# Kernel optimization log

Measured on AMD Instinct MI355X. Metric: run time of the kernel, lower is better.

Reference implementation:

```python
import jax, jax.numpy as jnp
import numpy as np

EPS = 1e-5
GROUPS = 4
KSZ = 3
PAD = 1
CUTON = 0.1


def conv1x1(x, w):
    # x: [b,c,h,w], w: [o,c,1,1]
    return jnp.einsum('bchw,oc->bohw', x, w[:, :, 0, 0])


def bn_eval(x, g, b, m, v):
    scale = g / jnp.sqrt(v + EPS)
    return (x - m[None, :, None, None]) * scale[None, :, None, None] + b[None, :, None, None]


def extract_patches(xp, k):
    # xp: [b,c,H+2p,W+2p] -> [b,c,h,w,k,k] (matches torch unfold(2,k,1).unfold(3,k,1))
    h = xp.shape[2] - k + 1
    w = xp.shape[3] - k + 1
    p = jnp.stack([xp[:, :, i:i + h, j:j + w] for i in range(k) for j in range(k)], axis=-1)
    return p.reshape(p.shape[:-1] + (k, k))


def batch_fftshift(z):
    # faithful to roll_n with n = d//2 (+1 if odd), over dims 1..3; roll_n == roll by -n
    for ax in (1, 2, 3):
        d = z.shape[ax]
        z = jnp.roll(z, -(d // 2 + (d % 2)), axis=ax)
    return z


def batch_ifftshift(z):
    for ax in (3, 2, 1):
        z = jnp.roll(z, -(z.shape[ax] // 2), axis=ax)
    return z


def attention_conv(x, yq, q_w, k_w, v_w, rel_h, rel_w):
    b, c, h, w = x.shape
    C = q_w.shape[0]
    px = jnp.pad(x, ((0, 0), (0, 0), (PAD, PAD), (PAD, PAD)))
    q = conv1x1(yq, q_w)                      # [b,C,h,w]
    k = conv1x1(px, k_w)
    v = conv1x1(px, v_w)
    kp = extract_patches(k, KSZ)              # [b,C,h,w,3,3]
    vp = extract_patches(v, KSZ)
    kh, kw = kp[:, :C // 2], kp[:, C // 2:]
    kp = jnp.concatenate([kh + rel_h, kw + rel_w], axis=1)
    kp = kp.reshape(b, GROUPS, C // GROUPS, h, w, KSZ * KSZ)
    vp = vp.reshape(b, GROUPS, C // GROUPS, h, w, KSZ * KSZ)
    q = q.reshape(b, GROUPS, C // GROUPS, h, w, 1)
    attn = jax.nn.softmax(q * kp, axis=-1)
    out = jnp.einsum('bgchwk,bgchwk->bgchw', attn, vp)
    return out.reshape(b, C, h, w)


def fam(x, rate1, rate2, w1, w0_w, w0_b):
    h, w = x.shape[2], x.shape[3]
    # torch.fft.fftn with dim=None -> FFT over ALL dims (batch & channel too)
    x_ft = jnp.fft.fftn(x, norm='ortho')
    out_ft = jnp.einsum('bixy,ioxy->boxy', x_ft, w1)
    s = batch_fftshift(out_ft)
    cy, cx = h // 2, w // 2
    rh, rw = int(CUTON * cy), int(CUTON * cx)
    mask = jnp.ones((h, w), dtype=x.dtype).at[cy - rh:cy + rh, cx - rw:cx + rw].set(0.0)
    s = s * mask
    out_ft = batch_ifftshift(s)
    # torch.fft.ifftn with s=(h,w) -> inverse FFT over last two dims only
    out = jnp.fft.ifftn(out_ft, s=(h, w), norm='ortho').real
    out2 = conv1x1(x, w0_w) + w0_b[None, :, None, None]
    return rate1 * out + rate2 * out2


def setup_inputs() -> dict:
    key = jax.random.key(0)
    ks = jax.random.split(key, 16)
    B, Cx, Cy, M, O, H, W = 4, 128, 256, 128, 128, 64, 64
    scale = 1.0 / (M * O)
    inp = {
        'x': jax.random.normal(ks[0], (B, Cx, H, W), jnp.float32),
        'y': jax.random.normal(ks[1], (B, Cy, H // 2, W // 2), jnp.float32),
        'conv1_w': jax.random.normal(ks[2], (M, Cy, 1, 1), jnp.float32) * 0.05,
        'bn1_g': jnp.ones((M,), jnp.float32),
        'bn1_b': jnp.zeros((M,), jnp.float32),
        'bn1_m': jnp.zeros((M,), jnp.float32),
        'bn1_v': jnp.ones((M,), jnp.float32),
        'q_w': jax.random.normal(ks[3], (M, M, 1, 1), jnp.float32) * 0.05,
        'k_w': jax.random.normal(ks[4], (M, M, 1, 1), jnp.float32) * 0.05,
        'v_w': jax.random.normal(ks[5], (M, M, 1, 1), jnp.float32) * 0.05,
        'rel_h': jax.random.normal(ks[6], (M // 2, 1, 1, 3, 1), jnp.float32),
        'rel_w': jax.random.normal(ks[7], (M // 2, 1, 1, 1, 3), jnp.float32),
        'rate1': jnp.full((1,), 0.5, jnp.float32),
        'rate2': jnp.full((1,), 0.5, jnp.float32),
        'w1_real': scale * jax.random.uniform(ks[8], (M, O, H, W), jnp.float32),
        'w1_imag': scale * jax.random.uniform(ks[9], (M, O, H, W), jnp.float32),
        'w0_w': jax.random.normal(ks[10], (O, M, 1, 1), jnp.float32) * 0.05,
        'w0_b': jnp.zeros((O,), jnp.float32),
        'bn2_g': jnp.ones((O,), jnp.float32),
        'bn2_b': jnp.zeros((O,), jnp.float32),
        'bn2_m': jnp.zeros((O,), jnp.float32),
        'bn2_v': jnp.ones((O,), jnp.float32),
    }
    return inp


def reference(x, y, conv1_w, bn1_g, bn1_b, bn1_m, bn1_v, q_w, k_w, v_w, rel_h, rel_w,
              rate1, rate2, w1_real, w1_imag, w0_w, w0_b, bn2_g, bn2_b, bn2_m, bn2_v):
    # conv1 (teacher proj) + BN + ReLU
    y1 = jax.nn.relu(bn_eval(conv1x1(y, conv1_w), bn1_g, bn1_b, bn1_m, bn1_v))
    # nearest interpolate to x spatial size (torch 'nearest': idx = floor(i*in/out))
    H, W = x.shape[2], x.shape[3]
    ih = (jnp.arange(H) * y1.shape[2]) // H
    iw = (jnp.arange(W) * y1.shape[3]) // W
    y_up = y1[:, :, ih][:, :, :, iw]
    # local unfold attention
    x_att = attention_conv(x, y_up, q_w, k_w, v_w, rel_h, rel_w)
    # FAM spectral branch + BN + ReLU
    w1 = jax.lax.complex(w1_real, w1_imag)
    y_out = jax.nn.relu(bn_eval(fam(x_att, rate1, rate2, w1, w0_w, w0_b),
                                bn2_g, bn2_b, bn2_m, bn2_v))
    return (y_out, x_att)
```

## Files before the change

### kernel.cpp

```cpp
#include <hip/hip_runtime.h>

#define BB 4
#define CY 256
#define CM 128
#define HW 4096
#define HWy 1024
#define PHW 4356
#define EPSF 1e-5f
#define TWOPI 6.2831853071795864769f

struct c32 { float re, im; };


__global__ void conv1_kernel(const float* __restrict__ y, const float* __restrict__ w,
                             const float* __restrict__ g, const float* __restrict__ bb,
                             const float* __restrict__ m, const float* __restrict__ v,
                             float* __restrict__ y1){
  int p = blockIdx.x*256 + threadIdx.x;
  int ocb = blockIdx.y*8;
  int b = blockIdx.z;
  float acc[8] = {0,0,0,0,0,0,0,0};
  const float* yb = y + (size_t)b*CY*HWy + p;
  #pragma unroll 4
  for(int ic=0; ic<CY; ic++){
    float xv = yb[(size_t)ic*HWy];
    #pragma unroll
    for(int j=0;j<8;j++) acc[j] += xv * w[(ocb+j)*CY + ic];
  }
  #pragma unroll
  for(int j=0;j<8;j++){
    int oc = ocb+j;
    float s = g[oc]*rsqrtf(v[oc]+EPSF);
    float bi = bb[oc] - m[oc]*s;
    float r = acc[j]*s + bi;
    y1[((size_t)(b*CM+oc))*HWy + p] = r>0.f?r:0.f;
  }
}

__global__ void qconv_kernel(const float* __restrict__ y1, const float* __restrict__ w,
                             float* __restrict__ q){
  int p = blockIdx.x*256 + threadIdx.x;
  int ocb = blockIdx.y*8; int b = blockIdx.z;
  int mi = ((p>>7)<<5) + ((p&63)>>1);
  float acc[8] = {0,0,0,0,0,0,0,0};
  const float* yb = y1 + (size_t)b*CM*HWy + mi;
  #pragma unroll 4
  for(int ic=0; ic<CM; ic++){
    float xv = yb[(size_t)ic*HWy];
    #pragma unroll
    for(int j=0;j<8;j++) acc[j] += xv * w[(ocb+j)*CM+ic];
  }
  #pragma unroll
  for(int j=0;j<8;j++) q[((size_t)(b*CM+ocb+j))*HW + p] = acc[j];
}

__global__ void kvconv_kernel(const float* __restrict__ x, const float* __restrict__ kw,
                              const float* __restrict__ vw,
                              float* __restrict__ k, float* __restrict__ v){
  int p = blockIdx.x*256 + threadIdx.x;
  int ocb = blockIdx.y*8; int b = blockIdx.z;
  if(p >= PHW) return;
  int hh = p/66, ww2 = p - hh*66;
  int ih = hh-1, iw = ww2-1;
  bool inb = (ih>=0 && ih<64 && iw>=0 && iw<64);
  float acck[8] = {0,0,0,0,0,0,0,0};
  float accv[8] = {0,0,0,0,0,0,0,0};
  if(inb){
    const float* xb = x + (size_t)b*CM*HW + ih*64 + iw;
    #pragma unroll 4
    for(int ic=0; ic<CM; ic++){
      float xv = xb[(size_t)ic*HW];
      #pragma unroll
      for(int j=0;j<8;j++){ acck[j] += xv*kw[(ocb+j)*CM+ic]; accv[j] += xv*vw[(ocb+j)*CM+ic]; }
    }
  }
  #pragma unroll
  for(int j=0;j<8;j++){
    size_t o = ((size_t)(b*CM+ocb+j))*PHW + p;
    k[o]=acck[j]; v[o]=accv[j];
  }
}


__global__ void attn_kernel(const float* __restrict__ q, const float* __restrict__ k,
                            const float* __restrict__ v, const float* __restrict__ relh,
                            const float* __restrict__ relw, float* __restrict__ xatt){
  int t = blockIdx.x*256 + threadIdx.x;
  int p = t & 4095;
  int bc = t >> 12;
  int c = bc & 127;
  int h = p>>6, w2 = p&63;
  float qv = q[(size_t)bc*HW + p];
  const float* kb = k + (size_t)bc*PHW;
  const float* vb = v + (size_t)bc*PHW;
  float lg[9], vv[9];
  #pragma unroll
  for(int ti=0; ti<3; ti++){
    #pragma unroll
    for(int tj=0; tj<3; tj++){
      int idx = (h+ti)*66 + (w2+tj);
      float rel = (c<64) ? relh[c*3+ti] : relw[(c-64)*3+tj];
      float kv = kb[idx] + rel;
      lg[ti*3+tj] = qv*kv;
      vv[ti*3+tj] = vb[idx];
    }
  }
  float mx = lg[0];
  #pragma unroll
  for(int i=1;i<9;i++) mx = fmaxf(mx, lg[i]);
  float s=0.f, o=0.f;
  #pragma unroll
  for(int i=0;i<9;i++){ float e = __expf(lg[i]-mx); s += e; o += e*vv[i]; }
  xatt[t] = o/s;
}


template<int SIGN>
__device__ inline void dft8(const c32* a, c32* X){
  constexpr float C8[8] = {1.f,0.70710678118654752f,0.f,-0.70710678118654752f,
                           -1.f,-0.70710678118654752f,0.f,0.70710678118654752f};
  constexpr float S8[8] = {0.f,0.70710678118654752f,1.f,0.70710678118654752f,
                           0.f,-0.70710678118654752f,-1.f,-0.70710678118654752f};
  #pragma unroll
  for(int kk=0;kk<8;kk++){
    float xr=0.f, xi=0.f;
    #pragma unroll
    for(int n=0;n<8;n++){
      const int j=(n*kk)&7;
      const float wr = C8[j];
      const float wi = SIGN*S8[j];
      xr += a[n].re*wr - a[n].im*wi;
      xi += a[n].re*wi + a[n].im*wr;
    }
    X[kk].re=xr; X[kk].im=xi;
  }
}

template<int SIGN, bool RIN, bool ROUT>
__global__ void fft64_kernel(const float* in, float* out,
                             int l_div, int s1, int s2, int estride, float scale){
  __shared__ c32 tmp[32][65];
  int ll = threadIdx.x & 31;
  int j  = threadIdx.x >> 5;
  int l = blockIdx.x*32 + ll;
  int base = (l/l_div)*s1 + (l%l_div)*s2;
  c32 a[8];
  #pragma unroll
  for(int n1=0;n1<8;n1++){
    int e = n1*8 + j;
    if(RIN){ a[n1].re = in[base + e*estride]; a[n1].im = 0.f; }
    else { const float2* ci = (const float2*)in; float2 t2 = ci[base + e*estride]; a[n1].re=t2.x; a[n1].im=t2.y; }
  }
  c32 A[8];
  dft8<SIGN>(a, A);
  #pragma unroll
  for(int k1=0;k1<8;k1++){
    float ang = SIGN * (TWOPI/64.f) * (float)(j*k1);
    float sn, cs; __sincosf(ang, &sn, &cs);
    c32 t; t.re = A[k1].re*cs - A[k1].im*sn; t.im = A[k1].re*sn + A[k1].im*cs;
    tmp[ll][k1*8+j] = t;
  }
  __syncthreads();
  c32 bv[8];
  #pragma unroll
  for(int n2=0;n2<8;n2++) bv[n2] = tmp[ll][j*8+n2];
  c32 Y[8];
  dft8<SIGN>(bv, Y);
  #pragma unroll
  for(int k2=0;k2<8;k2++){
    int e = j + 8*k2;
    int oi = base + e*estride;
    if(ROUT) out[oi] = Y[k2].re*scale;
    else { float2* co = (float2*)out; co[oi] = make_float2(Y[k2].re*scale, Y[k2].im*scale); }
  }
}

template<int SIGN>
__global__ void fft128_kernel(float* data, float scale){
  __shared__ c32 tmp[16][129];
  int ll = threadIdx.x & 15;
  int j  = threadIdx.x >> 4;
  int l = blockIdx.x*16 + ll;
  int b = l >> 12;
  int rem = l & 4095;
  size_t base = (size_t)b*CM*HW + rem;
  float2* cd = (float2*)data;
  c32 a[8];
  #pragma unroll
  for(int n1=0;n1<8;n1++){
    float2 t2 = cd[base + (size_t)(16*n1 + j)*HW];
    a[n1].re=t2.x; a[n1].im=t2.y;
  }
  c32 A[8];
  dft8<SIGN>(a, A);
  #pragma unroll
  for(int k1=0;k1<8;k1++){
    float ang = SIGN*(TWOPI/128.f)*(float)(j*k1);
    float sn,cs; __sincosf(ang,&sn,&cs);
    c32 t; t.re = A[k1].re*cs - A[k1].im*sn; t.im = A[k1].re*sn + A[k1].im*cs;
    tmp[ll][k1*16 + j] = t;
  }
  __syncthreads();
  int k1 = j & 7, half = j >> 3;
  c32 bv[16];
  #pragma unroll
  for(int n2=0;n2<16;n2++) bv[n2] = tmp[ll][k1*16+n2];
  #pragma unroll
  for(int kk=0;kk<8;kk++){
    int k2 = half*8 + kk;
    float xr=0.f, xi=0.f;
    #pragma unroll
    for(int n2=0;n2<16;n2++){
      float ang = SIGN*(TWOPI/16.f)*(float)((n2*k2)&15);
      float sn,cs; __sincosf(ang,&sn,&cs);
      xr += bv[n2].re*cs - bv[n2].im*sn;
      xi += bv[n2].re*sn + bv[n2].im*cs;
    }
    cd[base + (size_t)(k1 + 8*k2)*HW] = make_float2(xr*scale, xi*scale);
  }
}

__global__ void einsum_kernel(const float2* __restrict__ Xf, const float* __restrict__ w1r,
                              const float* __restrict__ w1i, float2* __restrict__ OutF){
  int fl = threadIdx.x & 63;
  int ol = threadIdx.x >> 6;
  int fbase = blockIdx.y*64;
  int obase = blockIdx.x*16;
  int f = fbase + fl;
  __shared__ float2 xs[4][64];
  c32 acc[4][4];
  #pragma unroll
  for(int a1=0;a1<4;a1++)
    #pragma unroll
    for(int a2=0;a2<4;a2++){ acc[a1][a2].re=0.f; acc[a1][a2].im=0.f; }
  for(int i=0;i<CM;i++){
    __syncthreads();
    xs[ol][fl] = Xf[((size_t)(ol*CM + i))*HW + f];
    __syncthreads();
    float2 x0=xs[0][fl], x1=xs[1][fl], x2=xs[2][fl], x3=xs[3][fl];
    c32 Xb[4];
    Xb[0].re = x0.x+x1.x+x2.x+x3.x;      Xb[0].im = x0.y+x1.y+x2.y+x3.y;
    Xb[1].re = x0.x + x1.y - x2.x - x3.y; Xb[1].im = x0.y - x1.x - x2.y + x3.x;
    Xb[2].re = x0.x - x1.x + x2.x - x3.x; Xb[2].im = x0.y - x1.y + x2.y - x3.y;
    Xb[3].re = x0.x - x1.y - x2.x + x3.y; Xb[3].im = x0.y + x1.x - x2.y - x3.x;
    #pragma unroll
    for(int oj=0;oj<4;oj++){
      int o = obase + oj*4 + ol;
      size_t wi_ = ((size_t)(i*CM + o))*HW + f;
      float wr = w1r[wi_], wim = w1i[wi_];
      #pragma unroll
      for(int kb=0;kb<4;kb++){
        acc[oj][kb].re += Xb[kb].re*wr - Xb[kb].im*wim;
        acc[oj][kb].im += Xb[kb].re*wim + Xb[kb].im*wr;
      }
    }
  }
  int hf = f>>6, wf = f&63;
  bool masked = (hf<3 || hf>60) && (wf<3 || wf>60);
  #pragma unroll
  for(int oj=0;oj<4;oj++){
    int o = obase + oj*4 + ol;
    #pragma unroll
    for(int kb=0;kb<4;kb++){
      float2 t2 = masked ? make_float2(0.f,0.f) : make_float2(acc[oj][kb].re, acc[oj][kb].im);
      OutF[((size_t)(kb*CM + o))*HW + f] = t2;
    }
  }
}

__global__ void final_kernel(const float* __restrict__ G, const float* __restrict__ xatt,
                             const float* __restrict__ w0, const float* __restrict__ w0b,
                             const float* __restrict__ r1p, const float* __restrict__ r2p,
                             const float* __restrict__ g2, const float* __restrict__ b2,
                             const float* __restrict__ m2, const float* __restrict__ v2,
                             float* __restrict__ yout){
  int p = blockIdx.x*256 + threadIdx.x;
  int ocb = blockIdx.y*8; int b = blockIdx.z;
  float r1 = r1p[0], r2 = r2p[0];
  float acc[8] = {0,0,0,0,0,0,0,0};
  const float* xb = xatt + (size_t)b*CM*HW + p;
  #pragma unroll 4
  for(int ic=0; ic<CM; ic++){
    float xv = xb[(size_t)ic*HW];
    #pragma unroll
    for(int j=0;j<8;j++) acc[j] += xv * w0[(ocb+j)*CM + ic];
  }
  #pragma unroll
  for(int j=0;j<8;j++){
    int oc = ocb+j;
    float fam = r1 * G[((size_t)(b*CM+oc))*HW + p] + r2*(acc[j] + w0b[oc]);
    float s = g2[oc]*rsqrtf(v2[oc]+EPSF);
    float bi = b2[oc] - m2[oc]*s;
    float val = fam*s + bi;
    yout[((size_t)(b*CM+oc))*HW + p] = val>0.f?val:0.f;
  }
}

extern "C" void kernel_launch(void* const* d_in, const int* in_sizes, int n_in,
                              void* d_out, int out_size, void* d_ws, size_t ws_size,
                              hipStream_t stream){
  const float* x       = (const float*)d_in[0];
  const float* y       = (const float*)d_in[1];
  const float* conv1_w = (const float*)d_in[2];
  const float* bn1_g   = (const float*)d_in[3];
  const float* bn1_b   = (const float*)d_in[4];
  const float* bn1_m   = (const float*)d_in[5];
  const float* bn1_v   = (const float*)d_in[6];
  const float* q_w     = (const float*)d_in[7];
  const float* k_w     = (const float*)d_in[8];
  const float* v_w     = (const float*)d_in[9];
  const float* rel_h   = (const float*)d_in[10];
  const float* rel_w   = (const float*)d_in[11];
  const float* rate1   = (const float*)d_in[12];
  const float* rate2   = (const float*)d_in[13];
  const float* w1r     = (const float*)d_in[14];
  const float* w1i     = (const float*)d_in[15];
  const float* w0_w    = (const float*)d_in[16];
  const float* w0_b    = (const float*)d_in[17];
  const float* bn2_g   = (const float*)d_in[18];
  const float* bn2_b   = (const float*)d_in[19];
  const float* bn2_m   = (const float*)d_in[20];
  const float* bn2_v   = (const float*)d_in[21];
  (void)in_sizes; (void)n_in; (void)out_size; (void)ws_size;

  char* ws = (char*)d_ws;
  float* Y1 = (float*)(ws + 0);
  float* Q  = (float*)(ws + 2097152);
  float* K  = (float*)(ws + 10485760);
  float* V  = (float*)(ws + 19406848);
  float2* E = (float2*)(ws + 0);
  float2* F = (float2*)(ws + 16777216);
  float*  G = (float*)(ws + 0);

  float* yout = (float*)d_out;
  float* xatt = (float*)d_out + 2097152;

  conv1_kernel<<<dim3(4,16,BB),256,0,stream>>>(y, conv1_w, bn1_g,bn1_b,bn1_m,bn1_v, Y1);
  qconv_kernel<<<dim3(16,16,BB),256,0,stream>>>(Y1, q_w, Q);
  kvconv_kernel<<<dim3(18,16,BB),256,0,stream>>>(x, k_w, v_w, K, V);
  attn_kernel<<<dim3(8192),256,0,stream>>>(Q, K, V, rel_h, rel_w, xatt);

  fft64_kernel<-1,true,false><<<dim3(1024),256,0,stream>>>(xatt, (float*)E, 64,4096,64, 1, 0.125f);
  fft64_kernel<-1,false,false><<<dim3(1024),256,0,stream>>>((float*)E, (float*)E, 64,4096,1, 64, 0.125f);
  fft128_kernel<-1><<<dim3(1024),256,0,stream>>>((float*)E, 0.044194173824159216f);
  einsum_kernel<<<dim3(8,64),256,0,stream>>>(E, w1r, w1i, F);
  fft64_kernel<1,false,false><<<dim3(1024),256,0,stream>>>((float*)F, (float*)F, 64,4096,1, 64, 0.125f);
  fft64_kernel<1,false,true><<<dim3(1024),256,0,stream>>>((float*)F, G, 64,4096,64, 1, 0.125f);

  final_kernel<<<dim3(16,16,BB),256,0,stream>>>(G, xatt, w0_w, w0_b, rate1, rate2,
                                                bn2_g,bn2_b,bn2_m,bn2_v, yout);
}
```

Measured before the change: 784.1 us.

## Fuse q-projection into attention, fuse 2D FFT passes in LDS, retile einsum

Removes the separate q-conv kernel by computing the q projection inside the attention kernel. Replaces the two separate 64-point FFT passes (forward and inverse) with one kernel per image that does both row and column FFTs in shared memory, saving global round trips. Rewrites the spectral einsum so each thread covers 4 frequencies with float4 weight loads and an 8-channel staged tile of the batch-FFT'd inputs. In exchange, attention now redoes 128-wide q dot products per thread, and the in-LDS FFT adds more syncthreads and possible bank conflicts on the strided column pass.

```diff
diff --git a/kernel.cpp b/kernel.cpp
--- a/kernel.cpp
+++ b/kernel.cpp
@@ -8,8 +8,6 @@
 #define PHW 4356
 #define EPSF 1e-5f
 #define TWOPI 6.2831853071795864769f
-
-struct c32 { float re, im; };
 
 
 __global__ void conv1_kernel(const float* __restrict__ y, const float* __restrict__ w,
@@ -35,23 +33,6 @@
     float r = acc[j]*s + bi;
     y1[((size_t)(b*CM+oc))*HWy + p] = r>0.f?r:0.f;
   }
-}
-
-__global__ void qconv_kernel(const float* __restrict__ y1, const float* __restrict__ w,
-                             float* __restrict__ q){
-  int p = blockIdx.x*256 + threadIdx.x;
-  int ocb = blockIdx.y*8; int b = blockIdx.z;
-  int mi = ((p>>7)<<5) + ((p&63)>>1);
-  float acc[8] = {0,0,0,0,0,0,0,0};
-  const float* yb = y1 + (size_t)b*CM*HWy + mi;
-  #pragma unroll 4
-  for(int ic=0; ic<CM; ic++){
-    float xv = yb[(size_t)ic*HWy];
-    #pragma unroll
-    for(int j=0;j<8;j++) acc[j] += xv * w[(ocb+j)*CM+ic];
-  }
-  #pragma unroll
-  for(int j=0;j<8;j++) q[((size_t)(b*CM+ocb+j))*HW + p] = acc[j];
 }
 
 __global__ void kvconv_kernel(const float* __restrict__ x, const float* __restrict__ kw,
@@ -82,15 +63,23 @@
 }
 
 
-__global__ void attn_kernel(const float* __restrict__ q, const float* __restrict__ k,
-                            const float* __restrict__ v, const float* __restrict__ relh,
-                            const float* __restrict__ relw, float* __restrict__ xatt){
+__global__ void attn_kernel(const float* __restrict__ y1, const float* __restrict__ qw,
+                            const float* __restrict__ k, const float* __restrict__ v,
+                            const float* __restrict__ relh, const float* __restrict__ relw,
+                            float* __restrict__ xatt){
   int t = blockIdx.x*256 + threadIdx.x;
   int p = t & 4095;
   int bc = t >> 12;
   int c = bc & 127;
+  int b = bc >> 7;
   int h = p>>6, w2 = p&63;
-  float qv = q[(size_t)bc*HW + p];
+  int mi = ((p>>7)<<5) + ((p&63)>>1);
+  const float* yb = y1 + (size_t)b*CM*HWy + mi;
+  const float* wq = qw + c*CM;
+  float qv = 0.f;
+  #pragma unroll 4
+  for(int ic=0; ic<CM; ic++) qv += yb[(size_t)ic*HWy] * wq[ic];
+
   const float* kb = k + (size_t)bc*PHW;
   const float* vb = v + (size_t)bc*PHW;
   float lg[9], vv[9];
@@ -116,7 +105,7 @@
 
 
 template<int SIGN>
-__device__ inline void dft8(const c32* a, c32* X){
+__device__ inline void dft8(const float2* a, float2* X){
   constexpr float C8[8] = {1.f,0.70710678118654752f,0.f,-0.70710678118654752f,
                            -1.f,-0.70710678118654752f,0.f,0.70710678118654752f};
   constexpr float S8[8] = {0.f,0.70710678118654752f,1.f,0.70710678118654752f,
@@ -129,55 +118,92 @@
       const int j=(n*kk)&7;
       const float wr = C8[j];
       const float wi = SIGN*S8[j];
-      xr += a[n].re*wr - a[n].im*wi;
-      xi += a[n].re*wi + a[n].im*wr;
-    }
-    X[kk].re=xr; X[kk].im=xi;
-  }
-}
-
-template<int SIGN, bool RIN, bool ROUT>
-__global__ void fft64_kernel(const float* in, float* out,
-                             int l_div, int s1, int s2, int estride, float scale){
-  __shared__ c32 tmp[32][65];
+      xr += a[n].x*wr - a[n].y*wi;
+      xi += a[n].x*wi + a[n].y*wr;
+    }
+    X[kk].x=xr; X[kk].y=xi;
+  }
+}
+
+template<int SIGN>
+__device__ inline void fft64_lds(float2* img, int lineStride, int elemStride){
+  int j  = threadIdx.x >> 5;
   int ll = threadIdx.x & 31;
-  int j  = threadIdx.x >> 5;
-  int l = blockIdx.x*32 + ll;
-  int base = (l/l_div)*s1 + (l%l_div)*s2;
-  c32 a[8];
-  #pragma unroll
-  for(int n1=0;n1<8;n1++){
-    int e = n1*8 + j;
-    if(RIN){ a[n1].re = in[base + e*estride]; a[n1].im = 0.f; }
-    else { const float2* ci = (const float2*)in; float2 t2 = ci[base + e*estride]; a[n1].re=t2.x; a[n1].im=t2.y; }
-  }
-  c32 A[8];
-  dft8<SIGN>(a, A);
-  #pragma unroll
-  for(int k1=0;k1<8;k1++){
-    float ang = SIGN * (TWOPI/64.f) * (float)(j*k1);
-    float sn, cs; __sincosf(ang, &sn, &cs);
-    c32 t; t.re = A[k1].re*cs - A[k1].im*sn; t.im = A[k1].re*sn + A[k1].im*cs;
-    tmp[ll][k1*8+j] = t;
+  #pragma unroll
+  for(int half=0; half<2; half++){
+    float2* L = img + (half*32 + ll)*lineStride;
+    float2 a[8];
+    #pragma unroll
+    for(int n1=0;n1<8;n1++) a[n1] = L[(n1*8+j)*elemStride];
+    float2 A[8];
+    dft8<SIGN>(a, A);
+    __syncthreads();
+    #pragma unroll
+    for(int k1=0;k1<8;k1++){
+      float ang = SIGN * (TWOPI/64.f) * (float)(j*k1);
+      float sn, cs; __sincosf(ang, &sn, &cs);
+      L[(k1*8+j)*elemStride] = make_float2(A[k1].x*cs - A[k1].y*sn, A[k1].x*sn + A[k1].y*cs);
+    }
+    __syncthreads();
+    float2 bv[8];
+    #pragma unroll
+    for(int n2=0;n2<8;n2++) bv[n2] = L[(j*8+n2)*elemStride];
+    float2 Y[8];
+    dft8<SIGN>(bv, Y);
+    __syncthreads();
+    #pragma unroll
+    for(int k2=0;k2<8;k2++) L[(j + 8*k2)*elemStride] = Y[k2];
+    __syncthreads();
+  }
+}
+
+__global__ void fft2d_fwd(const float* __restrict__ xatt, float2* __restrict__ E){
+  __shared__ float2 img[64*65];
+  int bc = blockIdx.x;
+  const float* src = xatt + (size_t)bc*HW;
+  for(int s=threadIdx.x; s<1024; s+=256){
+    float4 t = ((const float4*)src)[s];
+    int idx = s*4; int r = idx>>6, c = idx&63;
+    float2* d = img + r*65 + c;
+    d[0]=make_float2(t.x,0.f); d[1]=make_float2(t.y,0.f);
+    d[2]=make_float2(t.z,0.f); d[3]=make_float2(t.w,0.f);
   }
   __syncthreads();
-  c32 bv[8];
-  #pragma unroll
-  for(int n2=0;n2<8;n2++) bv[n2] = tmp[ll][j*8+n2];
-  c32 Y[8];
-  dft8<SIGN>(bv, Y);
-  #pragma unroll
-  for(int k2=0;k2<8;k2++){
-    int e = j + 8*k2;
-    int oi = base + e*estride;
-    if(ROUT) out[oi] = Y[k2].re*scale;
-    else { float2* co = (float2*)out; co[oi] = make_float2(Y[k2].re*scale, Y[k2].im*scale); }
+  fft64_lds<-1>(img, 65, 1);
+  fft64_lds<-1>(img, 1, 65);
+  float2* dst = E + (size_t)bc*HW;
+  for(int s=threadIdx.x; s<2048; s+=256){
+    int idx = s*2; int r = idx>>6, c = idx&63;
+    float2 v0 = img[r*65+c], v1 = img[r*65+c+1];
+    ((float4*)dst)[s] = make_float4(v0.x*0.015625f, v0.y*0.015625f, v1.x*0.015625f, v1.y*0.015625f);
+  }
+}
+
+__global__ void fft2d_inv(const float2* __restrict__ F, float* __restrict__ G){
+  __shared__ float2 img[64*65];
+  int bc = blockIdx.x;
+  const float2* src = F + (size_t)bc*HW;
+  for(int s=threadIdx.x; s<2048; s+=256){
+    float4 t = ((const float4*)src)[s];
+    int idx = s*2; int r = idx>>6, c = idx&63;
+    img[r*65+c]   = make_float2(t.x,t.y);
+    img[r*65+c+1] = make_float2(t.z,t.w);
+  }
+  __syncthreads();
+  fft64_lds<1>(img, 65, 1);
+  fft64_lds<1>(img, 1, 65);
+  float* dst = G + (size_t)bc*HW;
+  for(int s=threadIdx.x; s<1024; s+=256){
+    int idx = s*4; int r = idx>>6, c = idx&63;
+    float2* p2 = img + r*65 + c;
+    ((float4*)dst)[s] = make_float4(p2[0].x*0.015625f, p2[1].x*0.015625f,
+                                    p2[2].x*0.015625f, p2[3].x*0.015625f);
   }
 }
 
 template<int SIGN>
 __global__ void fft128_kernel(float* data, float scale){
-  __shared__ c32 tmp[16][129];
+  __shared__ float2 tmp[16][129];
   int ll = threadIdx.x & 15;
   int j  = threadIdx.x >> 4;
   int l = blockIdx.x*16 + ll;
@@ -185,24 +211,20 @@
   int rem = l & 4095;
   size_t base = (size_t)b*CM*HW + rem;
   float2* cd = (float2*)data;
-  c32 a[8];
-  #pragma unroll
-  for(int n1=0;n1<8;n1++){
-    float2 t2 = cd[base + (size_t)(16*n1 + j)*HW];
-    a[n1].re=t2.x; a[n1].im=t2.y;
-  }
-  c32 A[8];
+  float2 a[8];
+  #pragma unroll
+  for(int n1=0;n1<8;n1++) a[n1] = cd[base + (size_t)(16*n1 + j)*HW];
+  float2 A[8];
   dft8<SIGN>(a, A);
   #pragma unroll
   for(int k1=0;k1<8;k1++){
     float ang = SIGN*(TWOPI/128.f)*(float)(j*k1);
     float sn,cs; __sincosf(ang,&sn,&cs);
-    c32 t; t.re = A[k1].re*cs - A[k1].im*sn; t.im = A[k1].re*sn + A[k1].im*cs;
-    tmp[ll][k1*16 + j] = t;
+    tmp[ll][k1*16 + j] = make_float2(A[k1].x*cs - A[k1].y*sn, A[k1].x*sn + A[k1].y*cs);
   }
   __syncthreads();
   int k1 = j & 7, half = j >> 3;
-  c32 bv[16];
+  float2 bv[16];
   #pragma unroll
   for(int n2=0;n2<16;n2++) bv[n2] = tmp[ll][k1*16+n2];
   #pragma unroll
@@ -213,8 +235,8 @@
     for(int n2=0;n2<16;n2++){
       float ang = SIGN*(TWOPI/16.f)*(float)((n2*k2)&15);
       float sn,cs; __sincosf(ang,&sn,&cs);
-      xr += bv[n2].re*cs - bv[n2].im*sn;
-      xi += bv[n2].re*sn + bv[n2].im*cs;
+      xr += bv[n2].x*cs - bv[n2].y*sn;
+      xi += bv[n2].x*sn + bv[n2].y*cs;
     }
     cd[base + (size_t)(k1 + 8*k2)*HW] = make_float2(xr*scale, xi*scale);
   }
@@ -222,49 +244,64 @@
 
 __global__ void einsum_kernel(const float2* __restrict__ Xf, const float* __restrict__ w1r,
                               const float* __restrict__ w1i, float2* __restrict__ OutF){
-  int fl = threadIdx.x & 63;
-  int ol = threadIdx.x >> 6;
-  int fbase = blockIdx.y*64;
-  int obase = blockIdx.x*16;
-  int f = fbase + fl;
-  __shared__ float2 xs[4][64];
-  c32 acc[4][4];
+  int fl = threadIdx.x & 15;
+  int ol = threadIdx.x >> 4;
+  int obase = blockIdx.x * 16;
+  int fbase = blockIdx.y * 64;
+  __shared__ float2 Xs[8][4][64];
+  float accr[4][4], acci[4][4];
   #pragma unroll
   for(int a1=0;a1<4;a1++)
     #pragma unroll
-    for(int a2=0;a2<4;a2++){ acc[a1][a2].re=0.f; acc[a1][a2].im=0.f; }
-  for(int i=0;i<CM;i++){
-    __syncthreads();
-    xs[ol][fl] = Xf[((size_t)(ol*CM + i))*HW + f];
-    __syncthreads();
-    float2 x0=xs[0][fl], x1=xs[1][fl], x2=xs[2][fl], x3=xs[3][fl];
-    c32 Xb[4];
-    Xb[0].re = x0.x+x1.x+x2.x+x3.x;      Xb[0].im = x0.y+x1.y+x2.y+x3.y;
-    Xb[1].re = x0.x + x1.y - x2.x - x3.y; Xb[1].im = x0.y - x1.x - x2.y + x3.x;
-    Xb[2].re = x0.x - x1.x + x2.x - x3.x; Xb[2].im = x0.y - x1.y + x2.y - x3.y;
-    Xb[3].re = x0.x - x1.y - x2.x + x3.y; Xb[3].im = x0.y + x1.x - x2.y - x3.x;
-    #pragma unroll
-    for(int oj=0;oj<4;oj++){
-      int o = obase + oj*4 + ol;
-      size_t wi_ = ((size_t)(i*CM + o))*HW + f;
-      float wr = w1r[wi_], wim = w1i[wi_];
+    for(int a2=0;a2<4;a2++){ accr[a1][a2]=0.f; acci[a1][a2]=0.f; }
+
+  for(int ic=0; ic<CM; ic+=8){
+    __syncthreads();
+    #pragma unroll
+    for(int s=threadIdx.x; s<512; s+=256){
+      int ii = s>>6, fo = s&63;
+      size_t base = ((size_t)(ic+ii))*HW + fbase + fo;
+      float2 x0 = Xf[base];
+      float2 x1 = Xf[base +  524288];
+      float2 x2 = Xf[base + 1048576];
+      float2 x3 = Xf[base + 1572864];
+      Xs[ii][0][fo] = make_float2(x0.x+x1.x+x2.x+x3.x,       x0.y+x1.y+x2.y+x3.y);
+      Xs[ii][1][fo] = make_float2(x0.x+x1.y-x2.x-x3.y,       x0.y-x1.x-x2.y+x3.x);
+      Xs[ii][2][fo] = make_float2(x0.x-x1.x+x2.x-x3.x,       x0.y-x1.y+x2.y-x3.y);
+      Xs[ii][3][fo] = make_float2(x0.x-x1.y-x2.x+x3.y,       x0.y+x1.x-x2.y-x3.x);
+    }
+    __syncthreads();
+    #pragma unroll
+    for(int ii=0; ii<8; ii++){
+      size_t wbase = ((size_t)((ic+ii)*CM + obase + ol))*HW + fbase + fl*4;
+      float4 wr = *(const float4*)(w1r + wbase);
+      float4 wi = *(const float4*)(w1i + wbase);
       #pragma unroll
-      for(int kb=0;kb<4;kb++){
-        acc[oj][kb].re += Xb[kb].re*wr - Xb[kb].im*wim;
-        acc[oj][kb].im += Xb[kb].re*wim + Xb[kb].im*wr;
+      for(int kb=0; kb<4; kb++){
+        const float4* xp = (const float4*)&Xs[ii][kb][0];
+        float4 xa = xp[fl*2], xb = xp[fl*2+1];
+        accr[0][kb] += xa.x*wr.x - xa.y*wi.x;  acci[0][kb] += xa.x*wi.x + xa.y*wr.x;
+        accr[1][kb] += xa.z*wr.y - xa.w*wi.y;  acci[1][kb] += xa.z*wi.y + xa.w*wr.y;
+        accr[2][kb] += xb.x*wr.z - xb.y*wi.z;  acci[2][kb] += xb.x*wi.z + xb.y*wr.z;
+        accr[3][kb] += xb.z*wr.w - xb.w*wi.w;  acci[3][kb] += xb.z*wi.w + xb.w*wr.w;
       }
     }
   }
-  int hf = f>>6, wf = f&63;
-  bool masked = (hf<3 || hf>60) && (wf<3 || wf>60);
-  #pragma unroll
-  for(int oj=0;oj<4;oj++){
-    int o = obase + oj*4 + ol;
-    #pragma unroll
-    for(int kb=0;kb<4;kb++){
-      float2 t2 = masked ? make_float2(0.f,0.f) : make_float2(acc[oj][kb].re, acc[oj][kb].im);
-      OutF[((size_t)(kb*CM + o))*HW + f] = t2;
-    }
+  int f0 = fbase + fl*4;
+  float msk[4];
+  #pragma unroll
+  for(int ff=0; ff<4; ff++){
+    int f = f0+ff, hf = f>>6, wf = f&63;
+    msk[ff] = ((hf<3||hf>60)&&(wf<3||wf>60)) ? 0.f : 1.f;
+  }
+  int o = obase + ol;
+  #pragma unroll
+  for(int kb=0; kb<4; kb++){
+    float4* dst = (float4*)(OutF + ((size_t)(kb*CM+o))*HW + f0);
+    dst[0] = make_float4(accr[0][kb]*msk[0], acci[0][kb]*msk[0],
+                         accr[1][kb]*msk[1], acci[1][kb]*msk[1]);
+    dst[1] = make_float4(accr[2][kb]*msk[2], acci[2][kb]*msk[2],
+                         accr[3][kb]*msk[3], acci[3][kb]*msk[3]);
   }
 }
 
@@ -325,9 +362,8 @@
 
   char* ws = (char*)d_ws;
   float* Y1 = (float*)(ws + 0);
-  float* Q  = (float*)(ws + 2097152);
-  float* K  = (float*)(ws + 10485760);
-  float* V  = (float*)(ws + 19406848);
+  float* K  = (float*)(ws + 2097152);
+  float* V  = (float*)(ws + 11018240);
   float2* E = (float2*)(ws + 0);
   float2* F = (float2*)(ws + 16777216);
   float*  G = (float*)(ws + 0);
@@ -336,16 +372,13 @@
   float* xatt = (float*)d_out + 2097152;
 
   conv1_kernel<<<dim3(4,16,BB),256,0,stream>>>(y, conv1_w, bn1_g,bn1_b,bn1_m,bn1_v, Y1);
-  qconv_kernel<<<dim3(16,16,BB),256,0,stream>>>(Y1, q_w, Q);
   kvconv_kernel<<<dim3(18,16,BB),256,0,stream>>>(x, k_w, v_w, K, V);
-  attn_kernel<<<dim3(8192),256,0,stream>>>(Q, K, V, rel_h, rel_w, xatt);
-
-  fft64_kernel<-1,true,false><<<dim3(1024),256,0,stream>>>(xatt, (float*)E, 64,4096,64, 1, 0.125f);
-  fft64_kernel<-1,false,false><<<dim3(1024),256,0,stream>>>((float*)E, (float*)E, 64,4096,1, 64, 0.125f);
+  attn_kernel<<<dim3(8192),256,0,stream>>>(Y1, q_w, K, V, rel_h, rel_w, xatt);
+
+  fft2d_fwd<<<dim3(512),256,0,stream>>>(xatt, E);
   fft128_kernel<-1><<<dim3(1024),256,0,stream>>>((float*)E, 0.044194173824159216f);
   einsum_kernel<<<dim3(8,64),256,0,stream>>>(E, w1r, w1i, F);
-  fft64_kernel<1,false,false><<<dim3(1024),256,0,stream>>>((float*)F, (float*)F, 64,4096,1, 64, 0.125f);
-  fft64_kernel<1,false,true><<<dim3(1024),256,0,stream>>>((float*)F, G, 64,4096,64, 1, 0.125f);
+  fft2d_inv<<<dim3(512),256,0,stream>>>(F, G);
 
   final_kernel<<<dim3(16,16,BB),256,0,stream>>>(G, xatt, w0_w, w0_b, rate1, rate2,
                                                 bn2_g,bn2_b,bn2_m,bn2_v, yout);
```

Result: slower. 1.094 ms (+39.5%).
